# Performance work log

Measured on AMD Instinct MI355X. Metric: run time of the kernel, lower is better.

The kernel has to match this reference:

```python
import jax, jax.numpy as jnp
import numpy as np

N = 50000      # nodes per graph
G = 5          # num_graphs
F = 128        # in_channels
E0 = 800000    # random edges (avg degree 16)
H1, C1 = 8, 8  # conv1: heads=8, out=8 -> concat 64
C2 = 16        # conv2: heads=1, out=out_channels
NEG_SLOPE = 0.2


def setup_inputs() -> dict:
    key = jax.random.key(0)
    ks = jax.random.split(key, 12)
    x = jax.random.normal(ks[0], (G, N, F), dtype=jnp.float32)
    er = jax.random.randint(ks[1], (G, 2, E0), 0, N, dtype=jnp.int32)
    loops = jnp.broadcast_to(jnp.arange(N, dtype=jnp.int32), (G, 2, N))
    edge_index = jnp.concatenate([er, loops], axis=-1)  # [G, 2, E0+N] with self loops
    s = 0.1
    W1 = jax.random.normal(ks[2], (F, H1 * C1), jnp.float32) * s
    a_src1 = jax.random.normal(ks[3], (H1, C1), jnp.float32) * s
    a_dst1 = jax.random.normal(ks[4], (H1, C1), jnp.float32) * s
    b1 = jnp.zeros((H1 * C1,), jnp.float32)
    W2 = jax.random.normal(ks[5], (H1 * C1, C2), jnp.float32) * s
    a_src2 = jax.random.normal(ks[6], (1, C2), jnp.float32) * s
    a_dst2 = jax.random.normal(ks[7], (1, C2), jnp.float32) * s
    b2 = jnp.zeros((C2,), jnp.float32)
    Wf = jax.random.normal(ks[8], (C2 * G, 2), jnp.float32) * s
    bf = jnp.zeros((2,), jnp.float32)
    return {"x": x, "edge_index": edge_index, "W1": W1, "a_src1": a_src1,
            "a_dst1": a_dst1, "b1": b1, "W2": W2, "a_src2": a_src2,
            "a_dst2": a_dst2, "b2": b2, "Wf": Wf, "bf": bf}


def gat_layer(x, src, dst, W, a_src, a_dst, b):
    # x: [N, Fin]; src/dst: [E]; W: [Fin, H*C]; a_src/a_dst: [H, C]; b: [H*C]
    H, C = a_src.shape
    h = (x @ W).reshape(-1, H, C)                       # [N, H, C]
    alpha_s = jnp.einsum('nhc,hc->nh', h, a_src)        # [N, H]
    alpha_d = jnp.einsum('nhc,hc->nh', h, a_dst)
    e = jax.nn.leaky_relu(alpha_s[src] + alpha_d[dst], NEG_SLOPE)  # [E, H]
    m = jax.ops.segment_max(e, dst, num_segments=N)     # per-target softmax (stable)
    ex = jnp.exp(e - m[dst])
    denom = jax.ops.segment_sum(ex, dst, num_segments=N)
    alpha = ex / (denom[dst] + 1e-16)                   # [E, H]
    out = jax.ops.segment_sum(alpha[:, :, None] * h[src], dst, num_segments=N)  # [N, H, C]
    return out.reshape(-1, H * C) + b


def reference(x, edge_index, W1, a_src1, a_dst1, b1, W2, a_src2, a_dst2, b2, Wf, bf):
    def per_graph(xg, eg):
        src, dst = eg[0], eg[1]  # messages flow source -> target (PyG convention)
        h = jax.nn.relu(gat_layer(xg, src, dst, W1, a_src1, a_dst1, b1))
        return gat_layer(h, src, dst, W2, a_src2, a_dst2, b2)  # [N, C2]
    x_seq = jax.vmap(per_graph)(x, edge_index)          # [G, N, C2]
    x_seq = jnp.transpose(x_seq, (1, 0, 2)).reshape(N, G * C2)
    return x_seq @ Wf + bf                               # [N, 2]
```

## Files before the change

kernel.cpp:

```cpp
#include <hip/hip_runtime.h>

constexpr int N_NODES = 50000;
constexpr int G = 5;
constexpr int E = 850000;
constexpr int GN = G * N_NODES;
constexpr int GE = G * E;
constexpr float SLOPE = 0.2f;

constexpr int NPB = 1024;
constexpr int NBUK = (GN + NPB - 1) / NPB;
constexpr int EPB = 4096;
constexpr int NBLK_E = (GE + EPB - 1) / EPB;

static __device__ __forceinline__ float lrelu(float e) {
    return e > 0.f ? e : SLOPE * e;
}
static __device__ __forceinline__ unsigned short f2h(float f) {
    union { _Float16 h; unsigned short u; } v;
    v.h = (_Float16)f;
    return v.u;
}
static __device__ __forceinline__ float h2f(unsigned short u) {
    union { unsigned short u; _Float16 h; } v;
    v.u = u;
    return (float)v.h;
}

__global__ __launch_bounds__(256) void k_hist(const int* __restrict__ ei,
                                              int* __restrict__ H) {
    __shared__ int hist[NBUK];
    const int t = threadIdx.x, bi = blockIdx.x;
    for (int j = t; j < NBUK; j += 256) hist[j] = 0;
    __syncthreads();
#pragma unroll
    for (int i = 0; i < 16; ++i) {
        int idx = bi * EPB + i * 256 + t;
        if (idx < GE) {
            int g = idx / E;
            int el = idx - g * E;
            int dst = ei[(size_t)g * 2 * E + E + el];
            atomicAdd(&hist[(g * N_NODES + dst) >> 10], 1);
        }
    }
    __syncthreads();
    for (int j = t; j < NBUK; j += 256) H[(size_t)bi * NBUK + j] = hist[j];
}

__global__ __launch_bounds__(256) void k_scanH(int* __restrict__ H,
                                               int* __restrict__ T) {
    __shared__ int s[256];
    const int t = threadIdx.x, b = blockIdx.x;
    int run = 0;
    for (int c = 0; c < NBLK_E; c += 256) {
        int bi = c + t;
        int v = (bi < NBLK_E) ? H[(size_t)bi * NBUK + b] : 0;
        s[t] = v;
        for (int off = 1; off < 256; off <<= 1) {
            __syncthreads();
            int u = (t >= off) ? s[t - off] : 0;
            __syncthreads();
            s[t] += u;
        }
        __syncthreads();
        int excl = s[t] - v;
        if (bi < NBLK_E) H[(size_t)bi * NBUK + b] = run + excl;
        run += s[255];
        __syncthreads();
    }
    if (t == 0) T[b] = run;
}

__global__ __launch_bounds__(256) void k_scanT(const int* __restrict__ T,
                                               int* __restrict__ base_g) {
    __shared__ int s[256];
    const int t = threadIdx.x;
    int v = (t < NBUK) ? T[t] : 0;
    s[t] = v;
    for (int off = 1; off < 256; off <<= 1) {
        __syncthreads();
        int u = (t >= off) ? s[t - off] : 0;
        __syncthreads();
        s[t] += u;
    }
    __syncthreads();
    if (t < NBUK) base_g[t] = s[t] - v;
    if (t == 0) base_g[NBUK] = s[255];
}

__global__ __launch_bounds__(256) void k_scatter(const int* __restrict__ ei,
                                                 const int* __restrict__ H,
                                                 const int* __restrict__ base_g,
                                                 int* __restrict__ tmp) {
    __shared__ int cnt[NBUK];
    __shared__ int off[NBUK];
    const int t = threadIdx.x, bi = blockIdx.x;
    for (int j = t; j < NBUK; j += 256) {
        cnt[j] = 0;
        off[j] = base_g[j] + H[(size_t)bi * NBUK + j];
    }
    __syncthreads();
#pragma unroll
    for (int i = 0; i < 16; ++i) {
        int idx = bi * EPB + i * 256 + t;
        if (idx < GE) {
            int g = idx / E;
            int el = idx - g * E;
            const int* eb = ei + (size_t)g * 2 * E;
            int src = eb[el];
            int dst = eb[E + el];
            int gdst = g * N_NODES + dst;
            int b = gdst >> 10;
            int rank = atomicAdd(&cnt[b], 1);
            tmp[off[b] + rank] = ((gdst & 1023) << 18) | (g * N_NODES + src);
        }
    }
}

__global__ __launch_bounds__(256) void k_build(const int* __restrict__ base_g,
                                               const int* __restrict__ tmp,
                                               int* __restrict__ rowptr,
                                               int* __restrict__ deg,
                                               int* __restrict__ csr) {
    __shared__ int degL[NPB];
    __shared__ int curL[NPB];
    __shared__ int s[256];
    const int t = threadIdx.x, b = blockIdx.x;
    const int n0 = b << 10;
    const int nn = min(NPB, GN - n0);
    const int s0 = base_g[b], s1 = base_g[b + 1];
#pragma unroll
    for (int i = 0; i < 4; ++i) degL[t * 4 + i] = 0;
    __syncthreads();
    for (int i = s0 + t; i < s1; i += 256)
        atomicAdd(&degL[tmp[i] >> 18], 1);
    __syncthreads();
    int j0 = t * 4;
    int d0 = degL[j0], d1 = degL[j0 + 1], d2 = degL[j0 + 2], d3 = degL[j0 + 3];
    int tsum = d0 + d1 + d2 + d3;
    s[t] = tsum;
    for (int off = 1; off < 256; off <<= 1) {
        __syncthreads();
        int u = (t >= off) ? s[t - off] : 0;
        __syncthreads();
        s[t] += u;
    }
    __syncthreads();
    int excl = s[t] - tsum;
    int p0 = excl, p1 = p0 + d0, p2 = p1 + d1, p3 = p2 + d2;
    curL[j0] = p0; curL[j0 + 1] = p1; curL[j0 + 2] = p2; curL[j0 + 3] = p3;
    if (j0     < nn) { rowptr[n0 + j0]     = s0 + p0; deg[n0 + j0]     = d0; }
    if (j0 + 1 < nn) { rowptr[n0 + j0 + 1] = s0 + p1; deg[n0 + j0 + 1] = d1; }
    if (j0 + 2 < nn) { rowptr[n0 + j0 + 2] = s0 + p2; deg[n0 + j0 + 2] = d2; }
    if (j0 + 3 < nn) { rowptr[n0 + j0 + 3] = s0 + p3; deg[n0 + j0 + 3] = d3; }
    __syncthreads();
    for (int i = s0 + t; i < s1; i += 256) {
        int e = tmp[i];
        int r = atomicAdd(&curL[e >> 18], 1);
        csr[s0 + r] = e & 0x3FFFF;
    }
}

__global__ __launch_bounds__(256) void k_gemm1(const float* __restrict__ x,
                                               const float* __restrict__ W1,
                                               const float* __restrict__ a_src,
                                               const float* __restrict__ a_dst,
                                               unsigned short* __restrict__ h1f,
                                               unsigned short* __restrict__ l1,
                                               float* __restrict__ ad1) {
    __shared__ float Bs[128][68];
    __shared__ float As[64][65];
    __shared__ float aS[64], aD[64];
    const int t = threadIdx.x;
    const int rowBase = blockIdx.x * 64;

    const float4* W14 = (const float4*)W1;
#pragma unroll
    for (int i = 0; i < 8; ++i) {
        int v = t + i * 256;
        int k = v >> 4;
        int c = (v & 15) << 2;
        float4 w = W14[v];
        Bs[k][c] = w.x; Bs[k][c + 1] = w.y; Bs[k][c + 2] = w.z; Bs[k][c + 3] = w.w;
    }
    if (t < 64) { aS[t] = a_src[t]; aD[t] = a_dst[t]; }

    const int tx = t & 15;
    const int ty = t >> 4;
    float acc[4][4] = {};
    const float4* x4 = (const float4*)x;

    for (int kc = 0; kc < 128; kc += 64) {
        __syncthreads();
#pragma unroll
        for (int i = 0; i < 4; ++i) {
            int v = t + i * 256;
            int r = v >> 4;
            int kq = v & 15;
            int row = rowBase + r;
            float4 a = make_float4(0.f, 0.f, 0.f, 0.f);
            if (row < GN) a = x4[row * 32 + (kc >> 2) + kq];
            int kk = kq << 2;
            As[kk][r] = a.x; As[kk + 1][r] = a.y; As[kk + 2][r] = a.z; As[kk + 3][r] = a.w;
        }
        __syncthreads();
#pragma unroll 8
        for (int k = 0; k < 64; ++k) {
            float a0 = As[k][ty * 4 + 0];
            float a1 = As[k][ty * 4 + 1];
            float a2 = As[k][ty * 4 + 2];
            float a3 = As[k][ty * 4 + 3];
            float4 b = *(const float4*)&Bs[kc + k][tx * 4];
            acc[0][0] += a0 * b.x; acc[0][1] += a0 * b.y; acc[0][2] += a0 * b.z; acc[0][3] += a0 * b.w;
            acc[1][0] += a1 * b.x; acc[1][1] += a1 * b.y; acc[1][2] += a1 * b.z; acc[1][3] += a1 * b.w;
            acc[2][0] += a2 * b.x; acc[2][1] += a2 * b.y; acc[2][2] += a2 * b.z; acc[2][3] += a2 * b.w;
            acc[3][0] += a3 * b.x; acc[3][1] += a3 * b.y; acc[3][2] += a3 * b.z; acc[3][3] += a3 * b.w;
        }
    }
    const int head = tx >> 1;
    const int coff = (tx & 1) * 4;
#pragma unroll
    for (int i = 0; i < 4; ++i) {
        int row = rowBase + ty * 4 + i;
        float as_p = acc[i][0] * aS[head * 8 + coff]     + acc[i][1] * aS[head * 8 + coff + 1]
                   + acc[i][2] * aS[head * 8 + coff + 2] + acc[i][3] * aS[head * 8 + coff + 3];
        float ad_p = acc[i][0] * aD[head * 8 + coff]     + acc[i][1] * aD[head * 8 + coff + 1]
                   + acc[i][2] * aD[head * 8 + coff + 2] + acc[i][3] * aD[head * 8 + coff + 3];
        as_p += __shfl_xor(as_p, 1);
        ad_p += __shfl_xor(ad_p, 1);
        if (row < GN) {
            ushort4 fv = make_ushort4(f2h(acc[i][0]), f2h(acc[i][1]), f2h(acc[i][2]), f2h(acc[i][3]));
            *(ushort4*)(h1f + (size_t)row * 64 + tx * 4) = fv;
            if ((tx & 1) == 0) {
                l1[(size_t)row * 8 + head] = f2h(as_p);
                ad1[row * 8 + head] = ad_p;
            }
        }
    }
}

__global__ __launch_bounds__(256) void k_layer1(const int* __restrict__ rowptr,
                                                const int* __restrict__ deg,
                                                const int* __restrict__ csr,
                                                const unsigned short* __restrict__ h1f,
                                                const unsigned short* __restrict__ l1,
                                                const float* __restrict__ ad1,
                                                unsigned short* __restrict__ out1h) {
    const int tt = threadIdx.x & 63;
    const int h  = tt & 7;
    const int es = (tt >> 3) & 3;
    const int d  = blockIdx.x * 8 + (threadIdx.x >> 5);

    const int start = rowptr[d];
    const int dg    = deg[d];
    const float ad  = ad1[d * 8 + h];

    const unsigned int* h1d = (const unsigned int*)h1f;
    float a0 = 0.f, a1 = 0.f, a2 = 0.f, a3 = 0.f;
    float a4 = 0.f, a5 = 0.f, a6 = 0.f, a7 = 0.f;
    float den = 0.f;

    for (int j = es; j < dg; j += 4) {
        int s = csr[start + j];
        float w = __expf(lrelu(h2f(l1[(size_t)s * 8 + h]) + ad));
        den += w;
        const uint4 gp = *(const uint4*)(h1d + (size_t)s * 32 + h * 4);
        a0 += w * h2f((unsigned short)(gp.x & 0xffff));
        a1 += w * h2f((unsigned short)(gp.x >> 16));
        a2 += w * h2f((unsigned short)(gp.y & 0xffff));
        a3 += w * h2f((unsigned short)(gp.y >> 16));
        a4 += w * h2f((unsigned short)(gp.z & 0xffff));
        a5 += w * h2f((unsigned short)(gp.z >> 16));
        a6 += w * h2f((unsigned short)(gp.w & 0xffff));
        a7 += w * h2f((unsigned short)(gp.w >> 16));
    }
    a0 += __shfl_xor(a0, 8);  a0 += __shfl_xor(a0, 16);
    a1 += __shfl_xor(a1, 8);  a1 += __shfl_xor(a1, 16);
    a2 += __shfl_xor(a2, 8);  a2 += __shfl_xor(a2, 16);
    a3 += __shfl_xor(a3, 8);  a3 += __shfl_xor(a3, 16);
    a4 += __shfl_xor(a4, 8);  a4 += __shfl_xor(a4, 16);
    a5 += __shfl_xor(a5, 8);  a5 += __shfl_xor(a5, 16);
    a6 += __shfl_xor(a6, 8);  a6 += __shfl_xor(a6, 16);
    a7 += __shfl_xor(a7, 8);  a7 += __shfl_xor(a7, 16);
    den += __shfl_xor(den, 8); den += __shfl_xor(den, 16);

    if (es == 0) {
        float inv = 1.f / (den + 1e-16f);
        unsigned int p0 = (unsigned int)f2h(a0 * inv) | ((unsigned int)f2h(a1 * inv) << 16);
        unsigned int p1 = (unsigned int)f2h(a2 * inv) | ((unsigned int)f2h(a3 * inv) << 16);
        unsigned int p2 = (unsigned int)f2h(a4 * inv) | ((unsigned int)f2h(a5 * inv) << 16);
        unsigned int p3 = (unsigned int)f2h(a6 * inv) | ((unsigned int)f2h(a7 * inv) << 16);
        *(uint4*)(out1h + (size_t)d * 64 + h * 8) = make_uint4(p0, p1, p2, p3);
    }
}

__global__ __launch_bounds__(256) void k_gemm2(const unsigned short* __restrict__ agg1,
                                               const float* __restrict__ b1,
                                               const float* __restrict__ W2,
                                               const float* __restrict__ a_src,
                                               const float* __restrict__ a_dst,
                                               unsigned short* __restrict__ h2r,
                                               float* __restrict__ ad2) {
    __shared__ float As[64][65];
    __shared__ float Bs[64][20];
    __shared__ float aS[16], aD[16];
    const int t = threadIdx.x;
    const int rowBase = blockIdx.x * 64;

    {
        int k = t >> 2, c = (t & 3) << 2;
        float4 w = ((const float4*)W2)[t];
        Bs[k][c] = w.x; Bs[k][c + 1] = w.y; Bs[k][c + 2] = w.z; Bs[k][c + 3] = w.w;
    }
    if (t < 16) { aS[t] = a_src[t]; aD[t] = a_dst[t]; }
    const ushort4* a4p = (const ushort4*)agg1;
    const float4* b14 = (const float4*)b1;
#pragma unroll
    for (int i = 0; i < 4; ++i) {
        int v = t + i * 256;
        int r = v >> 4;
        int kq = v & 15;
        int row = rowBase + r;
        float ax = 0.f, ay = 0.f, az = 0.f, aw = 0.f;
        if (row < GN) {
            ushort4 a = a4p[row * 16 + kq];
            float4 bb = b14[kq];
            ax = fmaxf(h2f(a.x) + bb.x, 0.f);
            ay = fmaxf(h2f(a.y) + bb.y, 0.f);
            az = fmaxf(h2f(a.z) + bb.z, 0.f);
            aw = fmaxf(h2f(a.w) + bb.w, 0.f);
        }
        int kk = kq << 2;
        As[kk][r] = ax; As[kk + 1][r] = ay; As[kk + 2][r] = az; As[kk + 3][r] = aw;
    }
    __syncthreads();
    const int r = t >> 2;
    const int cg = (t & 3) << 2;
    float acc0 = 0.f, acc1 = 0.f, acc2 = 0.f, acc3 = 0.f;
#pragma unroll 8
    for (int k = 0; k < 64; ++k) {
        float a = As[k][r];
        float4 b = *(const float4*)&Bs[k][cg];
        acc0 += a * b.x; acc1 += a * b.y; acc2 += a * b.z; acc3 += a * b.w;
    }
    float as_p = acc0 * aS[cg] + acc1 * aS[cg + 1] + acc2 * aS[cg + 2] + acc3 * aS[cg + 3];
    float ad_p = acc0 * aD[cg] + acc1 * aD[cg + 1] + acc2 * aD[cg + 2] + acc3 * aD[cg + 3];
    as_p += __shfl_xor(as_p, 1); as_p += __shfl_xor(as_p, 2);
    ad_p += __shfl_xor(ad_p, 1); ad_p += __shfl_xor(ad_p, 2);
    int row = rowBase + r;
    if (row < GN) {
        ushort4 fv = make_ushort4(f2h(acc0), f2h(acc1), f2h(acc2), f2h(acc3));
        *(ushort4*)(h2r + (size_t)row * 20 + cg) = fv;
        if ((t & 3) == 0) {
            h2r[(size_t)row * 20 + 16] = f2h(as_p);
            ad2[row] = ad_p;
        }
    }
}

__global__ __launch_bounds__(256) void k_layer2(const int* __restrict__ rowptr,
                                                const int* __restrict__ deg,
                                                const int* __restrict__ csr,
                                                const unsigned short* __restrict__ h2r,
                                                const float* __restrict__ ad2,
                                                float* __restrict__ out2) {
    int d = __builtin_amdgcn_readfirstlane(blockIdx.x * 4 + (threadIdx.x >> 6));
    int tt = threadIdx.x & 63;
    int p = tt & 7;
    int sub = tt >> 3;
    int start = rowptr[d];
    int dg = deg[d];
    float ad = ad2[d];
    int sv = csr[start + min(tt, dg - 1)];
    int full = min(dg, 64);
    float den = 0.f, accx = 0.f, accy = 0.f;
    for (int base = 0; base < full; base += 8) {
        int j = base + sub;
        bool val = j < full;
        int s = __shfl(sv, j < 64 ? j : 0);
        const unsigned short* r = h2r + (size_t)s * 20;
        float w = val ? __expf(lrelu(h2f(r[16]) + ad)) : 0.f;
        unsigned int gp = *(const unsigned int*)(r + p * 2);
        den += w;
        accx += w * h2f((unsigned short)(gp & 0xffff));
        accy += w * h2f((unsigned short)(gp >> 16));
    }
    for (int base = 64; base < dg; base += 8) {
        int j = base + sub;
        bool val = j < dg;
        int s = csr[start + (val ? j : 0)];
        const unsigned short* r = h2r + (size_t)s * 20;
        float w = val ? __expf(lrelu(h2f(r[16]) + ad)) : 0.f;
        unsigned int gp = *(const unsigned int*)(r + p * 2);
        den += w;
        accx += w * h2f((unsigned short)(gp & 0xffff));
        accy += w * h2f((unsigned short)(gp >> 16));
    }
    accx += __shfl_xor(accx, 8); accx += __shfl_xor(accx, 16); accx += __shfl_xor(accx, 32);
    accy += __shfl_xor(accy, 8); accy += __shfl_xor(accy, 16); accy += __shfl_xor(accy, 32);
    den  += __shfl_xor(den, 8);  den  += __shfl_xor(den, 16);  den  += __shfl_xor(den, 32);
    if (sub == 0) {
        float inv = 1.f / (den + 1e-16f);
        ((float2*)out2)[(size_t)d * 8 + p] = make_float2(accx * inv, accy * inv);
    }
}

__global__ __launch_bounds__(256) void k_final(const float* __restrict__ agg2,
                                               const float* __restrict__ b2,
                                               const float* __restrict__ Wf,
                                               const float* __restrict__ bf,
                                               float* __restrict__ out) {
    int n = blockIdx.x * 256 + threadIdx.x;
    if (n >= N_NODES) return;
    float o0 = bf[0], o1 = bf[1];
#pragma unroll
    for (int g = 0; g < G; ++g) {
        const float4* v4 = (const float4*)agg2 + (size_t)(g * N_NODES + n) * 4;
#pragma unroll
        for (int q = 0; q < 4; ++q) {
            float4 v = v4[q];
            float4 b = ((const float4*)b2)[q];
            v.x += b.x; v.y += b.y; v.z += b.z; v.w += b.w;
            int kb = g * 16 + q * 4;
            o0 += v.x * Wf[(kb + 0) * 2]     + v.y * Wf[(kb + 1) * 2]
                + v.z * Wf[(kb + 2) * 2]     + v.w * Wf[(kb + 3) * 2];
            o1 += v.x * Wf[(kb + 0) * 2 + 1] + v.y * Wf[(kb + 1) * 2 + 1]
                + v.z * Wf[(kb + 2) * 2 + 1] + v.w * Wf[(kb + 3) * 2 + 1];
        }
    }
    out[n * 2]     = o0;
    out[n * 2 + 1] = o1;
}

extern "C" void kernel_launch(void* const* d_in, const int* in_sizes, int n_in,
                              void* d_out, int out_size, void* d_ws, size_t ws_size,
                              hipStream_t stream) {
    const float* x      = (const float*)d_in[0];
    const int*   ei     = (const int*)d_in[1];
    const float* W1     = (const float*)d_in[2];
    const float* a_src1 = (const float*)d_in[3];
    const float* a_dst1 = (const float*)d_in[4];
    const float* b1     = (const float*)d_in[5];
    const float* W2     = (const float*)d_in[6];
    const float* a_src2 = (const float*)d_in[7];
    const float* a_dst2 = (const float*)d_in[8];
    const float* b2     = (const float*)d_in[9];
    const float* Wf     = (const float*)d_in[10];
    const float* bf     = (const float*)d_in[11];
    float* out = (float*)d_out;

    unsigned short* h1f = (unsigned short*)d_ws;
    unsigned short* l1  = h1f + (size_t)GN * 64;
    unsigned short* h2r = h1f;
    float* out2 = (float*)(h2r + (size_t)GN * 20);
    unsigned short* out1h = h1f + (size_t)GN * 72;
    float* ad1  = (float*)(out1h + (size_t)GN * 64);
    float* ad2  = ad1;
    int*   iws    = (int*)(ad1 + (size_t)GN * 8);
    int*   rowptr = iws;
    int*   deg    = rowptr + GN;
    int*   base_g = deg + GN;
    int*   T      = base_g + (NBUK + 1);
    int*   H      = T + NBUK;
    int*   tmp    = H + (size_t)NBLK_E * NBUK;
    int*   csr    = tmp + GE;

    k_hist   <<<NBLK_E, 256, 0, stream>>>(ei, H);
    k_scanH  <<<NBUK,   256, 0, stream>>>(H, T);
    k_scanT  <<<1,      256, 0, stream>>>(T, base_g);
    k_scatter<<<NBLK_E, 256, 0, stream>>>(ei, H, base_g, tmp);
    k_build  <<<NBUK,   256, 0, stream>>>(base_g, tmp, rowptr, deg, csr);

    k_gemm1  <<<(GN + 63) / 64, 256, 0, stream>>>(x, W1, a_src1, a_dst1, h1f, l1, ad1);
    k_layer1 <<<GN / 8, 256, 0, stream>>>(rowptr, deg, csr, h1f, l1, ad1, out1h);
    k_gemm2  <<<(GN + 63) / 64, 256, 0, stream>>>(out1h, b1, W2, a_src2, a_dst2, h2r, ad2);
    k_layer2 <<<GN / 4, 256, 0, stream>>>(rowptr, deg, csr, h2r, ad2, out2);
    k_final  <<<(N_NODES + 255) / 256, 256, 0, stream>>>(out2, b2, Wf, bf, out);
}
```

Measured before the change: 550.6 us.

## Compute first-layer projection with split-fp16 MFMA instead of FP32 FMA

Replaces the shared-memory FP32 SIMT GEMM for x@W1 with matrix-core MFMA 16x16x16 fp16 instructions, using a hi/lo split of both operands (three MFMAs per tile) to keep near-fp32 accuracy. W1 is pre-split and transposed into fp16 hi/lo buffers by a small new kernel, and x rows are loaded straight into registers with no LDS staging. The epilogue computes the attention dot products with cross-lane shuffles. It adds a kernel launch and tripled MFMA work, and it stores h1f with scalar fp16 writes where the old code used vectorized ones.

```diff
diff --git a/kernel.cpp b/kernel.cpp
--- a/kernel.cpp
+++ b/kernel.cpp
@@ -11,6 +11,10 @@
 constexpr int NBUK = (GN + NPB - 1) / NPB;
 constexpr int EPB = 4096;
 constexpr int NBLK_E = (GE + EPB - 1) / EPB;
+
+typedef _Float16 f16;
+typedef f16 f16x4 __attribute__((ext_vector_type(4)));
+typedef float f32x4 __attribute__((ext_vector_type(4)));
 
 static __device__ __forceinline__ float lrelu(float e) {
     return e > 0.f ? e : SLOPE * e;
@@ -160,79 +164,104 @@
     }
 }
 
+__global__ __launch_bounds__(256) void k_prepW(const float* __restrict__ W1,
+                                               f16* __restrict__ WhT,
+                                               f16* __restrict__ WlT) {
+    int t = blockIdx.x * 256 + threadIdx.x;
+    if (t >= 128 * 64) return;
+    int k = t & 127;
+    int n = t >> 7;
+    float w = W1[k * 64 + n];
+    f16 h = (f16)w;
+    WhT[n * 128 + k] = h;
+    WlT[n * 128 + k] = (f16)(w - (float)h);
+}
+
 __global__ __launch_bounds__(256) void k_gemm1(const float* __restrict__ x,
-                                               const float* __restrict__ W1,
+                                               const f16* __restrict__ WhT,
+                                               const f16* __restrict__ WlT,
                                                const float* __restrict__ a_src,
                                                const float* __restrict__ a_dst,
                                                unsigned short* __restrict__ h1f,
                                                unsigned short* __restrict__ l1,
                                                float* __restrict__ ad1) {
-    __shared__ float Bs[128][68];
-    __shared__ float As[64][65];
-    __shared__ float aS[64], aD[64];
     const int t = threadIdx.x;
-    const int rowBase = blockIdx.x * 64;
-
-    const float4* W14 = (const float4*)W1;
-#pragma unroll
-    for (int i = 0; i < 8; ++i) {
-        int v = t + i * 256;
-        int k = v >> 4;
-        int c = (v & 15) << 2;
-        float4 w = W14[v];
-        Bs[k][c] = w.x; Bs[k][c + 1] = w.y; Bs[k][c + 2] = w.z; Bs[k][c + 3] = w.w;
-    }
-    if (t < 64) { aS[t] = a_src[t]; aD[t] = a_dst[t]; }
-
-    const int tx = t & 15;
-    const int ty = t >> 4;
-    float acc[4][4] = {};
+    const int lane = t & 63;
+    const int wv = t >> 6;
+    const int ln15 = lane & 15;
+    const int q = lane >> 4;
+    const int rowBase = blockIdx.x * 128 + wv * 32;
+
     const float4* x4 = (const float4*)x;
-
-    for (int kc = 0; kc < 128; kc += 64) {
-        __syncthreads();
+    float4 araw[2][8];
+#pragma unroll
+    for (int m = 0; m < 2; ++m) {
+        int row = rowBase + m * 16 + ln15;
+        row = row < GN ? row : GN - 1;
+        const float4* xr = x4 + (size_t)row * 32 + q;
+#pragma unroll
+        for (int s = 0; s < 8; ++s)
+            araw[m][s] = xr[s * 4];
+    }
+
+    f32x4 acc[2][4];
+#pragma unroll
+    for (int m = 0; m < 2; ++m)
+#pragma unroll
+        for (int nt = 0; nt < 4; ++nt)
+            acc[m][nt] = (f32x4){0.f, 0.f, 0.f, 0.f};
+
+#pragma unroll
+    for (int s = 0; s < 8; ++s) {
+        f16x4 bh[4], bl[4];
+#pragma unroll
+        for (int nt = 0; nt < 4; ++nt) {
+            int col = nt * 16 + ln15;
+            int o = col * 128 + s * 16 + q * 4;
+            bh[nt] = *(const f16x4*)(WhT + o);
+            bl[nt] = *(const f16x4*)(WlT + o);
+        }
+#pragma unroll
+        for (int m = 0; m < 2; ++m) {
+            float4 r = araw[m][s];
+            f16 h0 = (f16)r.x, h1 = (f16)r.y, h2 = (f16)r.z, h3 = (f16)r.w;
+            f16x4 ah = {h0, h1, h2, h3};
+            f16x4 al = {(f16)(r.x - (float)h0), (f16)(r.y - (float)h1),
+                        (f16)(r.z - (float)h2), (f16)(r.w - (float)h3)};
+#pragma unroll
+            for (int nt = 0; nt < 4; ++nt) {
+                acc[m][nt] = __builtin_amdgcn_mfma_f32_16x16x16f16(ah, bh[nt], acc[m][nt], 0, 0, 0);
+                acc[m][nt] = __builtin_amdgcn_mfma_f32_16x16x16f16(al, bh[nt], acc[m][nt], 0, 0, 0);
+                acc[m][nt] = __builtin_amdgcn_mfma_f32_16x16x16f16(ah, bl[nt], acc[m][nt], 0, 0, 0);
+            }
+        }
+    }
+
+    float aSv[4], aDv[4];
+#pragma unroll
+    for (int nt = 0; nt < 4; ++nt) {
+        aSv[nt] = a_src[nt * 16 + ln15];
+        aDv[nt] = a_dst[nt * 16 + ln15];
+    }
+#pragma unroll
+    for (int m = 0; m < 2; ++m) {
 #pragma unroll
         for (int i = 0; i < 4; ++i) {
-            int v = t + i * 256;
-            int r = v >> 4;
-            int kq = v & 15;
-            int row = rowBase + r;
-            float4 a = make_float4(0.f, 0.f, 0.f, 0.f);
-            if (row < GN) a = x4[row * 32 + (kc >> 2) + kq];
-            int kk = kq << 2;
-            As[kk][r] = a.x; As[kk + 1][r] = a.y; As[kk + 2][r] = a.z; As[kk + 3][r] = a.w;
-        }
-        __syncthreads();
-#pragma unroll 8
-        for (int k = 0; k < 64; ++k) {
-            float a0 = As[k][ty * 4 + 0];
-            float a1 = As[k][ty * 4 + 1];
-            float a2 = As[k][ty * 4 + 2];
-            float a3 = As[k][ty * 4 + 3];
-            float4 b = *(const float4*)&Bs[kc + k][tx * 4];
-            acc[0][0] += a0 * b.x; acc[0][1] += a0 * b.y; acc[0][2] += a0 * b.z; acc[0][3] += a0 * b.w;
-            acc[1][0] += a1 * b.x; acc[1][1] += a1 * b.y; acc[1][2] += a1 * b.z; acc[1][3] += a1 * b.w;
-            acc[2][0] += a2 * b.x; acc[2][1] += a2 * b.y; acc[2][2] += a2 * b.z; acc[2][3] += a2 * b.w;
-            acc[3][0] += a3 * b.x; acc[3][1] += a3 * b.y; acc[3][2] += a3 * b.z; acc[3][3] += a3 * b.w;
-        }
-    }
-    const int head = tx >> 1;
-    const int coff = (tx & 1) * 4;
-#pragma unroll
-    for (int i = 0; i < 4; ++i) {
-        int row = rowBase + ty * 4 + i;
-        float as_p = acc[i][0] * aS[head * 8 + coff]     + acc[i][1] * aS[head * 8 + coff + 1]
-                   + acc[i][2] * aS[head * 8 + coff + 2] + acc[i][3] * aS[head * 8 + coff + 3];
-        float ad_p = acc[i][0] * aD[head * 8 + coff]     + acc[i][1] * aD[head * 8 + coff + 1]
-                   + acc[i][2] * aD[head * 8 + coff + 2] + acc[i][3] * aD[head * 8 + coff + 3];
-        as_p += __shfl_xor(as_p, 1);
-        ad_p += __shfl_xor(ad_p, 1);
-        if (row < GN) {
-            ushort4 fv = make_ushort4(f2h(acc[i][0]), f2h(acc[i][1]), f2h(acc[i][2]), f2h(acc[i][3]));
-            *(ushort4*)(h1f + (size_t)row * 64 + tx * 4) = fv;
-            if ((tx & 1) == 0) {
-                l1[(size_t)row * 8 + head] = f2h(as_p);
-                ad1[row * 8 + head] = ad_p;
+            int row = rowBase + m * 16 + q * 4 + i;
+            bool ok = row < GN;
+#pragma unroll
+            for (int nt = 0; nt < 4; ++nt) {
+                float v = acc[m][nt][i];
+                if (ok) h1f[(size_t)row * 64 + nt * 16 + ln15] = f2h(v);
+                float ps = v * aSv[nt];
+                float pd = v * aDv[nt];
+                ps += __shfl_xor(ps, 1); ps += __shfl_xor(ps, 2); ps += __shfl_xor(ps, 4);
+                pd += __shfl_xor(pd, 1); pd += __shfl_xor(pd, 2); pd += __shfl_xor(pd, 4);
+                if (ok && (ln15 & 7) == 0) {
+                    int head = nt * 2 + (ln15 >> 3);
+                    l1[(size_t)row * 8 + head] = f2h(ps);
+                    ad1[row * 8 + head] = pd;
+                }
             }
         }
     }
@@ -463,6 +492,9 @@
     int*   H      = T + NBUK;
     int*   tmp    = H + (size_t)NBLK_E * NBUK;
     int*   csr    = tmp + GE;
+    uintptr_t wp = ((uintptr_t)(csr + GE) + 15) & ~(uintptr_t)15;
+    f16* WhT = (f16*)wp;
+    f16* WlT = WhT + 64 * 128;
 
     k_hist   <<<NBLK_E, 256, 0, stream>>>(ei, H);
     k_scanH  <<<NBUK,   256, 0, stream>>>(H, T);
@@ -470,7 +502,8 @@
     k_scatter<<<NBLK_E, 256, 0, stream>>>(ei, H, base_g, tmp);
     k_build  <<<NBUK,   256, 0, stream>>>(base_g, tmp, rowptr, deg, csr);
 
-    k_gemm1  <<<(GN + 63) / 64, 256, 0, stream>>>(x, W1, a_src1, a_dst1, h1f, l1, ad1);
+    k_prepW  <<<32, 256, 0, stream>>>(W1, WhT, WlT);
+    k_gemm1  <<<(GN + 127) / 128, 256, 0, stream>>>(x, WhT, WlT, a_src1, a_dst1, h1f, l1, ad1);
     k_layer1 <<<GN / 8, 256, 0, stream>>>(rowptr, deg, csr, h1f, l1, ad1, out1h);
     k_gemm2  <<<(GN + 63) / 64, 256, 0, stream>>>(out1h, b1, W2, a_src2, a_dst2, h2r, ad2);
     k_layer2 <<<GN / 4, 256, 0, stream>>>(rowptr, deg, csr, h2r, ad2, out2);
```

Result: slower. 585.1 us (+6.3%).
